# Performance work log

Measured on AMD Instinct MI355X. Metric: run time of the kernel, lower is better.

Reference implementation:

```python
import jax, jax.numpy as jnp
import numpy as np

FFT_LEN = 512
HOP = 256
WIN_LEN = 1024


def setup_inputs() -> dict:
    key = jax.random.key(0)
    k1, k2 = jax.random.split(key)
    inputs = jax.random.normal(k1, (8, 514, 4000), dtype=jnp.float32)
    win = jax.random.uniform(k2, (WIN_LEN,), dtype=jnp.float32)
    return {"inputs": inputs, "win": win}


def reference(inputs, win):
    B, D, T = inputs.shape  # D == 514
    half = FFT_LEN // 2  # 256
    real = inputs[:, :half, :]            # [B,256,T]
    imag = inputs[:, half + 1:-1, :]      # [B,256,T]
    c = jax.lax.complex(real, imag)       # bins 0..255
    # conjugate-symmetric extension: bin 256 = 0, bins 257..511 = conj(bins 255..1)
    tail = jnp.conj(jnp.flip(c[:, 1:, :], axis=1))            # [B,255,T]
    zero = jnp.zeros_like(c[:, :1, :])
    spec = jnp.concatenate([c, zero, tail], axis=1)           # [B,512,T]
    # torch does fft over the freq axis and keeps the real part
    ifft_data = jnp.real(jnp.fft.fft(spec, axis=1)).astype(jnp.float32)  # [B,512,T]
    tmp = jnp.concatenate([ifft_data, ifft_data], axis=1)     # [B,1024,T]
    tmp = tmp * win[None, :, None] * 256.0
    # overlap-add via four shifted padded copies (faithful to the original)
    t1 = jnp.pad(tmp, ((0, 0), (0, 768), (0, 3)))
    t2 = jnp.pad(tmp, ((0, 0), (256, 512), (1, 2)))
    t3 = jnp.pad(tmp, ((0, 0), (512, 256), (2, 1)))
    t4 = jnp.pad(tmp, ((0, 0), (768, 0), (3, 0)))
    synbuf = t1 + t2 + t3 + t4                                # [B,1792,T+3]
    syn = synbuf[:, 768:1024, :-4]                            # [B,256,T-1]
    syn = jnp.flip(syn, axis=1)
    syn = jnp.transpose(syn, (0, 2, 1)).reshape(B, -1)        # [B,256*(T-1)]
    return syn
```

## Files before the change

### kernel.cpp

```cpp
#include <hip/hip_runtime.h>


typedef __attribute__((ext_vector_type(8))) short short8;
typedef __attribute__((ext_vector_type(8))) __bf16 bf16x8;
typedef __attribute__((ext_vector_type(4))) float floatx4;

__device__ inline short f2bf(float f) {
  unsigned u = __builtin_bit_cast(unsigned, f);
  u = (u + 0x7fffu + ((u >> 16) & 1u)) >> 16;
  return (short)(unsigned short)u;
}

#define PI_OVER_256 0.01227184630308513f

__global__ void build_m(short* __restrict__ M) {
  int idx = blockIdx.x * blockDim.x + threadIdx.x;
  int ntile = idx >> 10;
  int s = (idx >> 6) & 15;
  int lane = idx & 63;
  int n = ntile * 16 + (lane & 15);
  int kb = lane >> 4;
  short8 v;
#pragma unroll
  for (int e = 0; e < 8; e++) {
    int kap = s * 32 + kb * 8 + e;
    int gk = 2 * (kap & 255) + (kap >> 8);
    float val;
    if (gk == 0) {
      val = 1.0f;
    } else if (gk < 256) {
      int m = (n * gk) & 511;
      val = 2.0f * __cosf((float)m * PI_OVER_256);
    } else {
      int m = (n * (gk - 256)) & 511;
      val = 2.0f * __sinf((float)m * PI_OVER_256);
    }
    v[e] = f2bf(val);
  }
  ((short8*)M)[idx] = v;
}

__global__ __launch_bounds__(512) void gemm_ola(
    const float* __restrict__ in, const float* __restrict__ win,
    const short* __restrict__ M, float* __restrict__ out) {
  __shared__ short ldsX[64 * 512];

  const int tid = threadIdx.x;
  const int b = blockIdx.y;
  const int tile = blockIdx.x;
  const int c0 = 61 * tile - 3;

  {
    const int col = tid & 63;
    const int kc = tid >> 6;
    const int gc = c0 + col;
    const bool valid = (gc >= 0) & (gc < 4000);
    const float* src = in + (size_t)b * 514 * 4000 + gc;
#pragma unroll
    for (int i0 = 0; i0 < 64; i0 += 8) {
      short8 v;
#pragma unroll
      for (int j = 0; j < 8; j++) {
        int kap = kc * 64 + i0 + j;
        int gk = 2 * (kap & 255) + (kap >> 8);
        int row = (gk < 256) ? gk : gk + 1;
        float f = valid ? src[(size_t)row * 4000] : 0.0f;
        v[j] = f2bf(f);
      }
      int g = (kc * 64 + i0) >> 3;
      *(short8*)&ldsX[col * 512 + ((g ^ (col & 7)) << 3)] = v;
    }
  }
  __syncthreads();

  const int w = tid >> 6;
  const int lane = tid & 63;
  const int c = lane & 15;
  const int kb = lane >> 4;

  floatx4 accE[2][4] = {};
  floatx4 accO[2][4] = {};

  const short8* Mf = (const short8*)M;
  const int nt0 = 2 * w, nt1 = 2 * w + 1;

#pragma unroll
  for (int s = 0; s < 16; s++) {
    bf16x8 a0 = __builtin_bit_cast(bf16x8, Mf[(nt0 * 16 + s) * 64 + lane]);
    bf16x8 a1 = __builtin_bit_cast(bf16x8, Mf[(nt1 * 16 + s) * 64 + lane]);
    bf16x8 bq[4];
    const int g = 4 * s + kb;
#pragma unroll
    for (int q = 0; q < 4; q++) {
      int col = 16 * q + c;
      bq[q] = __builtin_bit_cast(
          bf16x8, *(const short8*)&ldsX[col * 512 + ((g ^ (col & 7)) << 3)]);
    }
#pragma unroll
    for (int q = 0; q < 4; q++) {
      if (s < 8) {
        accE[0][q] = __builtin_amdgcn_mfma_f32_16x16x32_bf16(a0, bq[q], accE[0][q], 0, 0, 0);
        accE[1][q] = __builtin_amdgcn_mfma_f32_16x16x32_bf16(a1, bq[q], accE[1][q], 0, 0, 0);
      } else {
        accO[0][q] = __builtin_amdgcn_mfma_f32_16x16x32_bf16(a0, bq[q], accO[0][q], 0, 0, 0);
        accO[1][q] = __builtin_amdgcn_mfma_f32_16x16x32_bf16(a1, bq[q], accO[1][q], 0, 0, 0);
      }
    }
  }

#pragma unroll
  for (int jt = 0; jt < 2; jt++)
#pragma unroll
    for (int q = 0; q < 4; q++) {
      floatx4 e = accE[jt][q], o = accO[jt][q];
      accE[jt][q] = e + o;
      accO[jt][q] = e - o;
    }

  const int rg = lane >> 4;
#pragma unroll
  for (int jt = 0; jt < 2; jt++) {
    const int j0 = 32 * w + 16 * jt;
    const int jr = j0 + rg * 4;
    const floatx4 w0   = *(const floatx4*)&win[jr];
    const floatx4 w256 = *(const floatx4*)&win[256 + jr];
    const floatx4 w512 = *(const floatx4*)&win[512 + jr];
    const floatx4 w768 = *(const floatx4*)&win[768 + jr];
#pragma unroll
    for (int q = 0; q < 4; q++) {
      const int qm = (q > 0) ? (q - 1) : 0;
      floatx4 y1, yh2, y3;
#pragma unroll
      for (int p = 0; p < 4; p++) {
        float a1 = __shfl(accE[jt][q][p], lane - 1, 64);
        float b1 = (q > 0) ? __shfl(accE[jt][qm][p], lane + 15, 64) : 0.0f;
        y1[p] = (c >= 1) ? a1 : b1;
        float a2 = __shfl(accO[jt][q][p], lane - 2, 64);
        float b2 = (q > 0) ? __shfl(accO[jt][qm][p], lane + 14, 64) : 0.0f;
        yh2[p] = (c >= 2) ? a2 : b2;
        float a3 = __shfl(accE[jt][q][p], lane - 3, 64);
        float b3 = (q > 0) ? __shfl(accE[jt][qm][p], lane + 13, 64) : 0.0f;
        y3[p] = (c >= 3) ? a3 : b3;
      }
      const int t = c0 + 16 * q + c;
      if ((16 * q + c) >= 3 && t <= 3998) {
        floatx4 v = accO[jt][q] * w768 + y1 * w512 + yh2 * w256 + y3 * w0;
        v = v * 256.0f;
        floatx4 o;
        o[0] = v[3]; o[1] = v[2]; o[2] = v[1]; o[3] = v[0];
        const int ibase = 252 - j0 - 4 * rg;
        *(floatx4*)&out[((size_t)b * 3999 + t) * 256 + ibase] = o;
      }
    }
  }
}

extern "C" void kernel_launch(void* const* d_in, const int* in_sizes, int n_in,
                              void* d_out, int out_size, void* d_ws, size_t ws_size,
                              hipStream_t stream) {
  const float* in = (const float*)d_in[0];
  const float* win = (const float*)d_in[1];
  float* out = (float*)d_out;
  short* M = (short*)d_ws;

  hipLaunchKernelGGL(build_m, dim3(64), dim3(256), 0, stream, M);
  hipLaunchKernelGGL(gemm_ola, dim3(66, 8), dim3(512), 0, stream, in, win, M, out);
}
```

Before: 130.3 us.

## Shrink time tile to 32 columns, swap MFMA operand roles, vectorize input loads

Cuts each block's time tile from 64 to 32 columns (28 useful outputs plus 4 halo), launching 143 blocks per batch instead of 66. The MFMA operand roles are swapped so time becomes the row dimension. The overlap-add shifts then become cross-row-group shuffles, and the DFT matrix fragments are prefetched one step ahead. Input loading switches to float4 vector loads over 4 adjacent time columns, and the 256x window scaling is folded into per-lane scalars. The trade-off is more halo recompute (4 of 32 columns), scalar rather than vector output stores, and more blocks, in exchange for more parallelism and smaller LDS use.

Result: faster. 120.9 us (-7.2%).

```diff
diff --git a/kernel.cpp b/kernel.cpp
--- a/kernel.cpp
+++ b/kernel.cpp
@@ -43,31 +43,38 @@
 __global__ __launch_bounds__(512) void gemm_ola(
     const float* __restrict__ in, const float* __restrict__ win,
     const short* __restrict__ M, float* __restrict__ out) {
-  __shared__ short ldsX[64 * 512];
+  __shared__ short ldsX[32 * 512];
 
   const int tid = threadIdx.x;
   const int b = blockIdx.y;
   const int tile = blockIdx.x;
-  const int c0 = 61 * tile - 3;
+  const int c0 = 28 * tile - 4;
 
   {
-    const int col = tid & 63;
-    const int kc = tid >> 6;
-    const int gc = c0 + col;
-    const bool valid = (gc >= 0) & (gc < 4000);
-    const float* src = in + (size_t)b * 514 * 4000 + gc;
+    const int cbase = 4 * (tid & 7);
+    const int kap0 = (tid >> 3) * 8;
+    const int gc = c0 + cbase;
+    floatx4 f[8];
+    if (gc >= 0 && gc <= 3996) {
+      const float* src = in + (size_t)b * 2056000 + gc;
 #pragma unroll
-    for (int i0 = 0; i0 < 64; i0 += 8) {
+      for (int j = 0; j < 8; j++) {
+        int kap = kap0 + j;
+        int gk = 2 * (kap & 255) + (kap >> 8);
+        int row = (gk < 256) ? gk : gk + 1;
+        f[j] = *(const floatx4*)(src + (size_t)row * 4000);
+      }
+    } else {
+#pragma unroll
+      for (int j = 0; j < 8; j++) f[j] = floatx4{0.f, 0.f, 0.f, 0.f};
+    }
+    const int g = kap0 >> 3;
+#pragma unroll
+    for (int cc = 0; cc < 4; cc++) {
       short8 v;
 #pragma unroll
-      for (int j = 0; j < 8; j++) {
-        int kap = kc * 64 + i0 + j;
-        int gk = 2 * (kap & 255) + (kap >> 8);
-        int row = (gk < 256) ? gk : gk + 1;
-        float f = valid ? src[(size_t)row * 4000] : 0.0f;
-        v[j] = f2bf(f);
-      }
-      int g = (kc * 64 + i0) >> 3;
+      for (int j = 0; j < 8; j++) v[j] = f2bf(f[j][cc]);
+      const int col = cbase + cc;
       *(short8*)&ldsX[col * 512 + ((g ^ (col & 7)) << 3)] = v;
     }
   }
@@ -77,79 +84,92 @@
   const int lane = tid & 63;
   const int c = lane & 15;
   const int kb = lane >> 4;
+  const int rg = kb;
 
-  floatx4 accE[2][4] = {};
-  floatx4 accO[2][4] = {};
+  floatx4 accE[2][2] = {};
+  floatx4 accO[2][2] = {};
 
   const short8* Mf = (const short8*)M;
-  const int nt0 = 2 * w, nt1 = 2 * w + 1;
+  const int J0 = 2 * w, J1 = 2 * w + 1;
+
+  bf16x8 cb0 = __builtin_bit_cast(bf16x8, Mf[(J0 * 16 + 0) * 64 + lane]);
+  bf16x8 cb1 = __builtin_bit_cast(bf16x8, Mf[(J1 * 16 + 0) * 64 + lane]);
 
 #pragma unroll
   for (int s = 0; s < 16; s++) {
-    bf16x8 a0 = __builtin_bit_cast(bf16x8, Mf[(nt0 * 16 + s) * 64 + lane]);
-    bf16x8 a1 = __builtin_bit_cast(bf16x8, Mf[(nt1 * 16 + s) * 64 + lane]);
-    bf16x8 bq[4];
+    bf16x8 nb0, nb1;
+    if (s < 15) {
+      nb0 = __builtin_bit_cast(bf16x8, Mf[(J0 * 16 + s + 1) * 64 + lane]);
+      nb1 = __builtin_bit_cast(bf16x8, Mf[(J1 * 16 + s + 1) * 64 + lane]);
+    }
     const int g = 4 * s + kb;
-#pragma unroll
-    for (int q = 0; q < 4; q++) {
-      int col = 16 * q + c;
-      bq[q] = __builtin_bit_cast(
-          bf16x8, *(const short8*)&ldsX[col * 512 + ((g ^ (col & 7)) << 3)]);
+    const int col0 = c;
+    const int col1 = 16 + c;
+    bf16x8 a0 = __builtin_bit_cast(
+        bf16x8, *(const short8*)&ldsX[col0 * 512 + ((g ^ (col0 & 7)) << 3)]);
+    bf16x8 a1 = __builtin_bit_cast(
+        bf16x8, *(const short8*)&ldsX[col1 * 512 + ((g ^ (col1 & 7)) << 3)]);
+    if (s < 8) {
+      accE[0][0] = __builtin_amdgcn_mfma_f32_16x16x32_bf16(a0, cb0, accE[0][0], 0, 0, 0);
+      accE[0][1] = __builtin_amdgcn_mfma_f32_16x16x32_bf16(a0, cb1, accE[0][1], 0, 0, 0);
+      accE[1][0] = __builtin_amdgcn_mfma_f32_16x16x32_bf16(a1, cb0, accE[1][0], 0, 0, 0);
+      accE[1][1] = __builtin_amdgcn_mfma_f32_16x16x32_bf16(a1, cb1, accE[1][1], 0, 0, 0);
+    } else {
+      accO[0][0] = __builtin_amdgcn_mfma_f32_16x16x32_bf16(a0, cb0, accO[0][0], 0, 0, 0);
+      accO[0][1] = __builtin_amdgcn_mfma_f32_16x16x32_bf16(a0, cb1, accO[0][1], 0, 0, 0);
+      accO[1][0] = __builtin_amdgcn_mfma_f32_16x16x32_bf16(a1, cb0, accO[1][0], 0, 0, 0);
+      accO[1][1] = __builtin_amdgcn_mfma_f32_16x16x32_bf16(a1, cb1, accO[1][1], 0, 0, 0);
     }
-#pragma unroll
-    for (int q = 0; q < 4; q++) {
-      if (s < 8) {
-        accE[0][q] = __builtin_amdgcn_mfma_f32_16x16x32_bf16(a0, bq[q], accE[0][q], 0, 0, 0);
-        accE[1][q] = __builtin_amdgcn_mfma_f32_16x16x32_bf16(a1, bq[q], accE[1][q], 0, 0, 0);
-      } else {
-        accO[0][q] = __builtin_amdgcn_mfma_f32_16x16x32_bf16(a0, bq[q], accO[0][q], 0, 0, 0);
-        accO[1][q] = __builtin_amdgcn_mfma_f32_16x16x32_bf16(a1, bq[q], accO[1][q], 0, 0, 0);
-      }
-    }
+    if (s < 15) { cb0 = nb0; cb1 = nb1; }
   }
 
 #pragma unroll
-  for (int jt = 0; jt < 2; jt++)
+  for (int jt = 0; jt < 2; jt++) {
+    const int J = 2 * w + jt;
+    const int j = 16 * J + c;
+    const float wv0 = 256.0f * win[768 + j];
+    const float wv1 = 256.0f * win[512 + j];
+    const float wv2 = 256.0f * win[256 + j];
+    const float wv3 = 256.0f * win[j];
+
+    floatx4 Y[2], Yh[2];
 #pragma unroll
-    for (int q = 0; q < 4; q++) {
-      floatx4 e = accE[jt][q], o = accO[jt][q];
-      accE[jt][q] = e + o;
-      accO[jt][q] = e - o;
+    for (int q = 0; q < 2; q++) {
+      Y[q] = accE[q][jt] + accO[q][jt];
+      Yh[q] = accE[q][jt] - accO[q][jt];
     }
 
-  const int rg = lane >> 4;
 #pragma unroll
-  for (int jt = 0; jt < 2; jt++) {
-    const int j0 = 32 * w + 16 * jt;
-    const int jr = j0 + rg * 4;
-    const floatx4 w0   = *(const floatx4*)&win[jr];
-    const floatx4 w256 = *(const floatx4*)&win[256 + jr];
-    const floatx4 w512 = *(const floatx4*)&win[512 + jr];
-    const floatx4 w768 = *(const floatx4*)&win[768 + jr];
+    for (int q = 0; q < 2; q++) {
+      const int qm = (q > 0) ? q - 1 : 0;
+      float yb[4], yhb[4];
 #pragma unroll
-    for (int q = 0; q < 4; q++) {
-      const int qm = (q > 0) ? (q - 1) : 0;
-      floatx4 y1, yh2, y3;
+      for (int p = 1; p < 4; p++) {
+        float ia = __shfl(Y[q][p], lane - 16, 64);
+        float pa = __shfl(Y[qm][p], lane + 48, 64);
+        yb[p] = (rg > 0) ? ia : pa;
+      }
+#pragma unroll
+      for (int p = 2; p < 4; p++) {
+        float ia = __shfl(Yh[q][p], lane - 16, 64);
+        float pa = __shfl(Yh[qm][p], lane + 48, 64);
+        yhb[p] = (rg > 0) ? ia : pa;
+      }
+      floatx4 v;
 #pragma unroll
       for (int p = 0; p < 4; p++) {
-        float a1 = __shfl(accE[jt][q][p], lane - 1, 64);
-        float b1 = (q > 0) ? __shfl(accE[jt][qm][p], lane + 15, 64) : 0.0f;
-        y1[p] = (c >= 1) ? a1 : b1;
-        float a2 = __shfl(accO[jt][q][p], lane - 2, 64);
-        float b2 = (q > 0) ? __shfl(accO[jt][qm][p], lane + 14, 64) : 0.0f;
-        yh2[p] = (c >= 2) ? a2 : b2;
-        float a3 = __shfl(accE[jt][q][p], lane - 3, 64);
-        float b3 = (q > 0) ? __shfl(accE[jt][qm][p], lane + 13, 64) : 0.0f;
-        y3[p] = (c >= 3) ? a3 : b3;
+        float t1 = (p >= 1) ? Y[q][p - 1] : yb[3];
+        float t2 = (p >= 2) ? Yh[q][p - 2] : yhb[p + 2];
+        float t3 = (p >= 3) ? Y[q][p - 3] : yb[p + 1];
+        v[p] = wv0 * Yh[q][p] + wv1 * t1 + wv2 * t2 + wv3 * t3;
       }
-      const int t = c0 + 16 * q + c;
-      if ((16 * q + c) >= 3 && t <= 3998) {
-        floatx4 v = accO[jt][q] * w768 + y1 * w512 + yh2 * w256 + y3 * w0;
-        v = v * 256.0f;
-        floatx4 o;
-        o[0] = v[3]; o[1] = v[2]; o[2] = v[1]; o[3] = v[0];
-        const int ibase = 252 - j0 - 4 * rg;
-        *(floatx4*)&out[((size_t)b * 3999 + t) * 256 + ibase] = o;
+#pragma unroll
+      for (int p = 0; p < 4; p++) {
+        const int L = 16 * q + 4 * rg + p;
+        const int t = c0 + L;
+        if (L >= 4 && t <= 3998) {
+          out[((size_t)b * 3999 + t) * 256 + (255 - j)] = v[p];
+        }
       }
     }
   }
@@ -164,5 +184,5 @@
   short* M = (short*)d_ws;
 
   hipLaunchKernelGGL(build_m, dim3(64), dim3(256), 0, stream, M);
-  hipLaunchKernelGGL(gemm_ola, dim3(66, 8), dim3(512), 0, stream, in, win, M, out);
+  hipLaunchKernelGGL(gemm_ola, dim3(143, 8), dim3(512), 0, stream, in, win, M, out);
 }
```
